# Optimization experiments

Measured on AMD Instinct MI355X. Metric: run time of the kernel, lower is better.

Reference implementation:

```python
import jax, jax.numpy as jnp
import numpy as np

N_NODES = 1_000_000
N_EDGES = 32_000_000
EPS_INIT = 100.0


def setup_inputs() -> dict:
    key = jax.random.key(0)
    ks = jax.random.split(key, 8)
    x = jax.random.normal(ks[0], (N_NODES, 1), dtype=jnp.float32)
    edge_index = jax.random.randint(ks[1], (2, N_EDGES), 0, N_NODES, dtype=jnp.int64)
    # MLP params: Linear(1,20) -> ReLU -> Linear(20,20) -> ReLU -> Linear(20,1)
    w1 = jax.random.normal(ks[2], (1, 20), dtype=jnp.float32) / np.sqrt(1.0)
    b1 = jnp.zeros((20,), dtype=jnp.float32)
    w2 = jax.random.normal(ks[3], (20, 20), dtype=jnp.float32) / np.sqrt(20.0)
    b2 = jnp.zeros((20,), dtype=jnp.float32)
    w3 = jax.random.normal(ks[4], (20, 1), dtype=jnp.float32) / np.sqrt(20.0)
    b3 = jnp.zeros((1,), dtype=jnp.float32)
    eps = jnp.asarray(EPS_INIT, dtype=jnp.float32)
    return {"x": x, "edge_index": edge_index, "eps": eps,
            "w1": w1, "b1": b1, "w2": w2, "b2": b2, "w3": w3, "b3": b3}


def reference(x, edge_index, eps, w1, b1, w2, b2, w3, b3):
    # GINConv: out = MLP((1 + eps) * x + sum_{j in N(i)} x_j)
    src, dst = edge_index[0], edge_index[1]
    # gather source features per edge, scatter-add to destination nodes
    agg = jax.ops.segment_sum(x[src], dst, num_segments=N_NODES)  # [N, 1]
    h = (1.0 + eps) * x + agg
    h = jax.nn.relu(h @ w1 + b1)   # [N, 20]
    h = jax.nn.relu(h @ w2 + b2)   # [N, 20]
    out = h @ w3 + b3              # [N, 1]
    return out
```

## Files before the change

kernel.cpp:

```cpp
#include <hip/hip_runtime.h>

#define N_NODES 1000000
#define N_EDGES 32000000

#define NB        256
#define TSC       1024
#define EPB       125000
#define QPB       31250
#define NBKT      245
#define BKT_PAD   256
#define CAP       135168
#define RING      96

#define BINS_ELEMS  ((size_t)NBKT * CAP)
#define CNT_ELEMS   ((size_t)NB * BKT_PAD)
#define PAGG_ELEMS  ((size_t)NBKT * 2 * 4096)
#define WS_NEEDED   ((BINS_ELEMS + CNT_ELEMS + BKT_PAD + PAGG_ELEMS) * 4)

__global__ __launch_bounds__(TSC) void gin_count(const int* __restrict__ dst,
                                                 unsigned* __restrict__ cnt) {
    __shared__ unsigned h[BKT_PAD];
    int tid = threadIdx.x;
    if (tid < BKT_PAD) h[tid] = 0u;
    __syncthreads();
    int k = blockIdx.x;
    const int4* q = reinterpret_cast<const int4*>(dst) + (size_t)k * QPB;
    for (int i = tid; i < QPB; i += TSC) {
        int4 d = q[i];
        atomicAdd(&h[d.x >> 12], 1u);
        atomicAdd(&h[d.y >> 12], 1u);
        atomicAdd(&h[d.z >> 12], 1u);
        atomicAdd(&h[d.w >> 12], 1u);
    }
    __syncthreads();
    if (tid < BKT_PAD) cnt[(size_t)k * BKT_PAD + tid] = h[tid];
}

__global__ void gin_scan(unsigned* __restrict__ cnt, unsigned* __restrict__ tot) {
    int gtid = blockIdx.x * blockDim.x + threadIdx.x;
    int b = gtid >> 6;
    int lane = gtid & 63;
    if (b >= BKT_PAD) return;
    unsigned running = 0;
    for (int base = 0; base < NB; base += 64) {
        int idx = base + lane;
        unsigned v = (idx < NB) ? cnt[(size_t)idx * BKT_PAD + b] : 0u;
        unsigned s = v;
        for (int d = 1; d < 64; d <<= 1) {
            unsigned u = __shfl_up(s, d);
            if (lane >= d) s += u;
        }
        unsigned excl = s - v;
        if (idx < NB) cnt[(size_t)idx * BKT_PAD + b] = running + excl;
        running += __shfl(s, 63);
    }
    if (lane == 0) tot[b] = running;
}

__global__ __launch_bounds__(TSC) void gin_scatter_bins(const int* __restrict__ src,
                                                        const int* __restrict__ dst,
                                                        const unsigned* __restrict__ cnt,
                                                        unsigned* __restrict__ bins) {
    __shared__ unsigned stage[BKT_PAD][RING];
    __shared__ unsigned stot[BKT_PAD];
    __shared__ unsigned sflt[BKT_PAD];
    __shared__ unsigned sbase[BKT_PAD];

    int tid = threadIdx.x;
    int k = blockIdx.x;
    if (tid < BKT_PAD) {
        stot[tid] = 0u;
        sflt[tid] = 0u;
        sbase[tid] = cnt[(size_t)k * BKT_PAD + tid];
    }
    __syncthreads();

    const int4* qs = reinterpret_cast<const int4*>(src) + (size_t)k * QPB;
    const int4* qd = reinterpret_cast<const int4*>(dst) + (size_t)k * QPB;

    for (int t0 = 0; t0 < QPB; t0 += TSC) {
        int i = t0 + tid;
        if (i < QPB) {
            int4 s4 = qs[i];
            int4 d4 = qd[i];
#define PUT(ss, dd) do {                                                     \
            unsigned b_ = (unsigned)(dd) >> 12;                              \
            unsigned p_ = atomicAdd(&stot[b_], 1u);                          \
            stage[b_][p_ % RING] =                                           \
                (((unsigned)(dd) & 4095u) << 20) | (unsigned)(ss);           \
        } while (0)
            PUT(s4.x, d4.x);
            PUT(s4.y, d4.y);
            PUT(s4.z, d4.z);
            PUT(s4.w, d4.w);
#undef PUT
        }
        __syncthreads();
        if (tid < BKT_PAD) {
            unsigned b = (unsigned)tid;
            unsigned T = stot[b];
            unsigned F = sflt[b];
            if (F + 32 <= T) {
                unsigned gbase = sbase[b];
                unsigned* gout = bins + (size_t)b * CAP;
                while (F + 32 <= T) {
                    unsigned r = F % RING;
                    unsigned gp = gbase + F;
                    if (gp + 32 <= CAP) {
#pragma unroll
                        for (int c = 0; c < 32; ++c) gout[gp + c] = stage[b][r + c];
                    }
                    F += 32;
                }
                sflt[b] = F;
            }
        }
        __syncthreads();
    }
    if (tid < BKT_PAD) {
        unsigned b = (unsigned)tid;
        unsigned T = stot[b];
        unsigned F = sflt[b];
        unsigned gbase = sbase[b];
        unsigned* gout = bins + (size_t)b * CAP;
        for (; F < T; ++F) {
            unsigned gp = gbase + F;
            if (gp < CAP) gout[gp] = stage[b][F % RING];
        }
    }
}

__global__ __launch_bounds__(1024) void gin_reduce(const unsigned* __restrict__ bins,
                                                   const unsigned* __restrict__ tot,
                                                   const float* __restrict__ x,
                                                   float* __restrict__ pagg) {
    __shared__ float acc[4096];
    int tid = threadIdx.x;
    int blk = blockIdx.x;
    int b = blk >> 1;
    int h = blk & 1;
    for (int i = tid; i < 4096; i += 1024) acc[i] = 0.0f;
    __syncthreads();

    unsigned n = tot[b];
    if (n > CAP) n = CAP;
    const unsigned* bb = bins + (size_t)b * CAP;
    const uint4* bb4 = reinterpret_cast<const uint4*>(bb);
    unsigned nq = n >> 2;
    unsigned q_lo = h ? (nq >> 1) : 0;
    unsigned q_hi = h ? nq : (nq >> 1);
    for (unsigned i = q_lo + tid; i < q_hi; i += 1024) {
        uint4 e = bb4[i];
        atomicAdd(&acc[e.x >> 20], x[e.x & 0xFFFFFu]);
        atomicAdd(&acc[e.y >> 20], x[e.y & 0xFFFFFu]);
        atomicAdd(&acc[e.z >> 20], x[e.z & 0xFFFFFu]);
        atomicAdd(&acc[e.w >> 20], x[e.w & 0xFFFFFu]);
    }
    if (h) {
        for (unsigned i = (nq << 2) + tid; i < n; i += 1024) {
            unsigned e = bb[i];
            atomicAdd(&acc[e >> 20], x[e & 0xFFFFFu]);
        }
    }
    __syncthreads();

    float* po = pagg + (size_t)blk * 4096;
    for (int i = tid; i < 4096; i += 1024) po[i] = acc[i];
}

__global__ __launch_bounds__(512) void gin_combine_mlp(const float* __restrict__ pagg,
                               const float* __restrict__ x,
                               const float* __restrict__ eps,
                               const float* __restrict__ w1,
                               const float* __restrict__ b1,
                               const float* __restrict__ w2,
                               const float* __restrict__ b2,
                               const float* __restrict__ w3,
                               const float* __restrict__ b3,
                               float* __restrict__ out) {
    int i = blockIdx.x * blockDim.x + threadIdx.x;
    if (i >= N_NODES) return;
    int b = i >> 12;
    int j = i & 4095;
    float agg = pagg[(size_t)(b * 2) * 4096 + j] + pagg[(size_t)(b * 2 + 1) * 4096 + j];
    float h0 = (1.0f + eps[0]) * x[i] + agg;

    float h1[20];
#pragma unroll
    for (int jj = 0; jj < 20; ++jj)
        h1[jj] = fmaxf(fmaf(h0, w1[jj], b1[jj]), 0.0f);

    float o = b3[0];
#pragma unroll
    for (int kk = 0; kk < 20; ++kk) {
        float a = b2[kk];
#pragma unroll
        for (int jj = 0; jj < 20; ++jj)
            a = fmaf(h1[jj], w2[jj * 20 + kk], a);
        o = fmaf(fmaxf(a, 0.0f), w3[kk], o);
    }
    out[i] = o;
}

__global__ void gin_zero_kernel(float* __restrict__ agg, int n) {
    int i = blockIdx.x * blockDim.x + threadIdx.x;
    if (i < n) agg[i] = 0.0f;
}

__global__ void gin_scatter_kernel(const float* __restrict__ x,
                                   const int* __restrict__ src,
                                   const int* __restrict__ dst,
                                   float* __restrict__ agg) {
    int q = blockIdx.x * blockDim.x + threadIdx.x;
    int e = q * 4;
    if (e + 3 < N_EDGES) {
        int4 s = *reinterpret_cast<const int4*>(src + e);
        int4 d = *reinterpret_cast<const int4*>(dst + e);
        atomicAdd(&agg[d.x], x[s.x]);
        atomicAdd(&agg[d.y], x[s.y]);
        atomicAdd(&agg[d.z], x[s.z]);
        atomicAdd(&agg[d.w], x[s.w]);
    } else if (e < N_EDGES) {
        for (; e < N_EDGES; ++e) atomicAdd(&agg[dst[e]], x[src[e]]);
    }
}

__global__ void gin_mlp_kernel(const float* __restrict__ x,
                               const float* __restrict__ agg,
                               const float* __restrict__ eps,
                               const float* __restrict__ w1,
                               const float* __restrict__ b1,
                               const float* __restrict__ w2,
                               const float* __restrict__ b2,
                               const float* __restrict__ w3,
                               const float* __restrict__ b3,
                               float* __restrict__ out) {
    int i = blockIdx.x * blockDim.x + threadIdx.x;
    if (i >= N_NODES) return;
    float h0 = (1.0f + eps[0]) * x[i] + agg[i];
    float h1[20];
#pragma unroll
    for (int j = 0; j < 20; ++j) h1[j] = fmaxf(fmaf(h0, w1[j], b1[j]), 0.0f);
    float o = b3[0];
#pragma unroll
    for (int k = 0; k < 20; ++k) {
        float a = b2[k];
#pragma unroll
        for (int j = 0; j < 20; ++j) a = fmaf(h1[j], w2[j * 20 + k], a);
        o = fmaf(fmaxf(a, 0.0f), w3[k], o);
    }
    out[i] = o;
}

extern "C" void kernel_launch(void* const* d_in, const int* in_sizes, int n_in,
                              void* d_out, int out_size, void* d_ws, size_t ws_size,
                              hipStream_t stream) {
    const float* x    = (const float*)d_in[0];
    const int*   ei   = (const int*)  d_in[1];
    const float* eps  = (const float*)d_in[2];
    const float* w1   = (const float*)d_in[3];
    const float* b1   = (const float*)d_in[4];
    const float* w2   = (const float*)d_in[5];
    const float* b2   = (const float*)d_in[6];
    const float* w3   = (const float*)d_in[7];
    const float* b3   = (const float*)d_in[8];
    float* out = (float*)d_out;

    const int* src = ei;
    const int* dst = ei + N_EDGES;

    if (ws_size >= WS_NEEDED) {
        unsigned* bins = (unsigned*)d_ws;
        unsigned* cnt  = bins + BINS_ELEMS;
        unsigned* tot  = cnt + CNT_ELEMS;
        float*    pagg = (float*)(tot + BKT_PAD);

        gin_count<<<NB, TSC, 0, stream>>>(dst, cnt);
        {
            int blocks = (BKT_PAD * 64 + 255) / 256;
            gin_scan<<<blocks, 256, 0, stream>>>(cnt, tot);
        }
        gin_scatter_bins<<<NB, TSC, 0, stream>>>(src, dst, cnt, bins);
        gin_reduce<<<NBKT * 2, 1024, 0, stream>>>(bins, tot, x, pagg);
        gin_combine_mlp<<<(N_NODES + 511) / 512, 512, 0, stream>>>(pagg, x, eps,
                                                 w1, b1, w2, b2, w3, b3, out);
    } else {
        float* agg = (ws_size >= (size_t)N_NODES * sizeof(float)) ? (float*)d_ws : out;
        {
            int blocks = (N_NODES + 255) / 256;
            gin_zero_kernel<<<blocks, 256, 0, stream>>>(agg, N_NODES);
        }
        {
            int quads = N_EDGES / 4;
            int blocks = (quads + 255) / 256;
            gin_scatter_kernel<<<blocks, 256, 0, stream>>>(x, src, dst, agg);
        }
        {
            int blocks = (N_NODES + 255) / 256;
            gin_mlp_kernel<<<blocks, 256, 0, stream>>>(x, agg, eps, w1, b1, w2, b2,
                                                       w3, b3, out);
        }
    }
}
```

Measured before the change: 408.6 us.

## Batch loads for memory-level parallelism, prefetch scatter input, pad LDS ring stride

The count kernel now issues four int4 loads per thread before doing its histogram atomics. The scatter kernel prefetches the next iteration's src/dst vectors across the sync barrier. Its staging ring rows are padded to a stride of 97 so the per-bucket flush reads, which walk row-wise across threads, avoid LDS bank conflicts. The reduce kernel batches four uint4 bin loads and sixteen x gathers before the LDS atomics to expose more outstanding memory requests, at the cost of higher register pressure.

```diff
diff --git a/kernel.cpp b/kernel.cpp
--- a/kernel.cpp
+++ b/kernel.cpp
@@ -11,11 +11,13 @@
 #define BKT_PAD   256
 #define CAP       135168
 #define RING      96
+#define RSTRIDE   97
 
 #define BINS_ELEMS  ((size_t)NBKT * CAP)
 #define CNT_ELEMS   ((size_t)NB * BKT_PAD)
 #define PAGG_ELEMS  ((size_t)NBKT * 2 * 4096)
 #define WS_NEEDED   ((BINS_ELEMS + CNT_ELEMS + BKT_PAD + PAGG_ELEMS) * 4)
+
 
 __global__ __launch_bounds__(TSC) void gin_count(const int* __restrict__ dst,
                                                  unsigned* __restrict__ cnt) {
@@ -25,12 +27,22 @@
     __syncthreads();
     int k = blockIdx.x;
     const int4* q = reinterpret_cast<const int4*>(dst) + (size_t)k * QPB;
-    for (int i = tid; i < QPB; i += TSC) {
-        int4 d = q[i];
-        atomicAdd(&h[d.x >> 12], 1u);
-        atomicAdd(&h[d.y >> 12], 1u);
-        atomicAdd(&h[d.z >> 12], 1u);
-        atomicAdd(&h[d.w >> 12], 1u);
+    for (int base = 0; base < QPB; base += TSC * 4) {
+        int i0 = base + tid, i1 = i0 + TSC, i2 = i1 + TSC, i3 = i2 + TSC;
+        int4 d0 = {0,0,0,0}, d1 = {0,0,0,0}, d2 = {0,0,0,0}, d3 = {0,0,0,0};
+        bool v0 = i0 < QPB, v1 = i1 < QPB, v2 = i2 < QPB, v3 = i3 < QPB;
+        if (v0) d0 = q[i0];
+        if (v1) d1 = q[i1];
+        if (v2) d2 = q[i2];
+        if (v3) d3 = q[i3];
+        if (v0) { atomicAdd(&h[d0.x >> 12], 1u); atomicAdd(&h[d0.y >> 12], 1u);
+                  atomicAdd(&h[d0.z >> 12], 1u); atomicAdd(&h[d0.w >> 12], 1u); }
+        if (v1) { atomicAdd(&h[d1.x >> 12], 1u); atomicAdd(&h[d1.y >> 12], 1u);
+                  atomicAdd(&h[d1.z >> 12], 1u); atomicAdd(&h[d1.w >> 12], 1u); }
+        if (v2) { atomicAdd(&h[d2.x >> 12], 1u); atomicAdd(&h[d2.y >> 12], 1u);
+                  atomicAdd(&h[d2.z >> 12], 1u); atomicAdd(&h[d2.w >> 12], 1u); }
+        if (v3) { atomicAdd(&h[d3.x >> 12], 1u); atomicAdd(&h[d3.y >> 12], 1u);
+                  atomicAdd(&h[d3.z >> 12], 1u); atomicAdd(&h[d3.w >> 12], 1u); }
     }
     __syncthreads();
     if (tid < BKT_PAD) cnt[(size_t)k * BKT_PAD + tid] = h[tid];
@@ -61,7 +73,7 @@
                                                         const int* __restrict__ dst,
                                                         const unsigned* __restrict__ cnt,
                                                         unsigned* __restrict__ bins) {
-    __shared__ unsigned stage[BKT_PAD][RING];
+    __shared__ unsigned stage[BKT_PAD][RSTRIDE];
     __shared__ unsigned stot[BKT_PAD];
     __shared__ unsigned sflt[BKT_PAD];
     __shared__ unsigned sbase[BKT_PAD];
@@ -78,21 +90,27 @@
     const int4* qs = reinterpret_cast<const int4*>(src) + (size_t)k * QPB;
     const int4* qd = reinterpret_cast<const int4*>(dst) + (size_t)k * QPB;
 
+    int4 s_cur = {0,0,0,0}, d_cur = {0,0,0,0};
+    bool v_cur = tid < QPB;
+    if (v_cur) { s_cur = qs[tid]; d_cur = qd[tid]; }
+
     for (int t0 = 0; t0 < QPB; t0 += TSC) {
-        int i = t0 + tid;
-        if (i < QPB) {
-            int4 s4 = qs[i];
-            int4 d4 = qd[i];
+        int nx = t0 + TSC + tid;
+        int4 s_nxt = {0,0,0,0}, d_nxt = {0,0,0,0};
+        bool v_nxt = nx < QPB;
+        if (v_nxt) { s_nxt = qs[nx]; d_nxt = qd[nx]; }
+
+        if (v_cur) {
 #define PUT(ss, dd) do {                                                     \
             unsigned b_ = (unsigned)(dd) >> 12;                              \
             unsigned p_ = atomicAdd(&stot[b_], 1u);                          \
             stage[b_][p_ % RING] =                                           \
                 (((unsigned)(dd) & 4095u) << 20) | (unsigned)(ss);           \
         } while (0)
-            PUT(s4.x, d4.x);
-            PUT(s4.y, d4.y);
-            PUT(s4.z, d4.z);
-            PUT(s4.w, d4.w);
+            PUT(s_cur.x, d_cur.x);
+            PUT(s_cur.y, d_cur.y);
+            PUT(s_cur.z, d_cur.z);
+            PUT(s_cur.w, d_cur.w);
 #undef PUT
         }
         __syncthreads();
@@ -116,6 +134,7 @@
             }
         }
         __syncthreads();
+        s_cur = s_nxt; d_cur = d_nxt; v_cur = v_nxt;
     }
     if (tid < BKT_PAD) {
         unsigned b = (unsigned)tid;
@@ -149,7 +168,31 @@
     unsigned nq = n >> 2;
     unsigned q_lo = h ? (nq >> 1) : 0;
     unsigned q_hi = h ? nq : (nq >> 1);
-    for (unsigned i = q_lo + tid; i < q_hi; i += 1024) {
+
+    unsigned i = q_lo + tid;
+    for (; i + 3072 < q_hi; i += 4096) {
+        uint4 e0 = bb4[i];
+        uint4 e1 = bb4[i + 1024];
+        uint4 e2 = bb4[i + 2048];
+        uint4 e3 = bb4[i + 3072];
+        float v0x = x[e0.x & 0xFFFFFu], v0y = x[e0.y & 0xFFFFFu];
+        float v0z = x[e0.z & 0xFFFFFu], v0w = x[e0.w & 0xFFFFFu];
+        float v1x = x[e1.x & 0xFFFFFu], v1y = x[e1.y & 0xFFFFFu];
+        float v1z = x[e1.z & 0xFFFFFu], v1w = x[e1.w & 0xFFFFFu];
+        float v2x = x[e2.x & 0xFFFFFu], v2y = x[e2.y & 0xFFFFFu];
+        float v2z = x[e2.z & 0xFFFFFu], v2w = x[e2.w & 0xFFFFFu];
+        float v3x = x[e3.x & 0xFFFFFu], v3y = x[e3.y & 0xFFFFFu];
+        float v3z = x[e3.z & 0xFFFFFu], v3w = x[e3.w & 0xFFFFFu];
+        atomicAdd(&acc[e0.x >> 20], v0x); atomicAdd(&acc[e0.y >> 20], v0y);
+        atomicAdd(&acc[e0.z >> 20], v0z); atomicAdd(&acc[e0.w >> 20], v0w);
+        atomicAdd(&acc[e1.x >> 20], v1x); atomicAdd(&acc[e1.y >> 20], v1y);
+        atomicAdd(&acc[e1.z >> 20], v1z); atomicAdd(&acc[e1.w >> 20], v1w);
+        atomicAdd(&acc[e2.x >> 20], v2x); atomicAdd(&acc[e2.y >> 20], v2y);
+        atomicAdd(&acc[e2.z >> 20], v2z); atomicAdd(&acc[e2.w >> 20], v2w);
+        atomicAdd(&acc[e3.x >> 20], v3x); atomicAdd(&acc[e3.y >> 20], v3y);
+        atomicAdd(&acc[e3.z >> 20], v3z); atomicAdd(&acc[e3.w >> 20], v3w);
+    }
+    for (; i < q_hi; i += 1024) {
         uint4 e = bb4[i];
         atomicAdd(&acc[e.x >> 20], x[e.x & 0xFFFFFu]);
         atomicAdd(&acc[e.y >> 20], x[e.y & 0xFFFFFu]);
@@ -157,15 +200,15 @@
         atomicAdd(&acc[e.w >> 20], x[e.w & 0xFFFFFu]);
     }
     if (h) {
-        for (unsigned i = (nq << 2) + tid; i < n; i += 1024) {
-            unsigned e = bb[i];
+        for (unsigned j = (nq << 2) + tid; j < n; j += 1024) {
+            unsigned e = bb[j];
             atomicAdd(&acc[e >> 20], x[e & 0xFFFFFu]);
         }
     }
     __syncthreads();
 
     float* po = pagg + (size_t)blk * 4096;
-    for (int i = tid; i < 4096; i += 1024) po[i] = acc[i];
+    for (int j = tid; j < 4096; j += 1024) po[j] = acc[j];
 }
 
 __global__ __launch_bounds__(512) void gin_combine_mlp(const float* __restrict__ pagg,
```

After: 407.0 us. No clear change (-0.4%).
